# Optimization experiments

Hardware: AMD Instinct MI355X
Metric: run time of the kernel (lower is better)

Reference implementation:

```python
import jax, jax.numpy as jnp
import numpy as np

N = 50000      # nodes
E = 800000     # edges (avg degree 16)
G = 128        # graphs in batch
IN = 128       # in_channels
H = 128        # hidden_dim
C = 10         # num_classes


def setup_inputs() -> dict:
    key = jax.random.key(0)
    ks = jax.random.split(key, 8)
    x = jax.random.normal(ks[0], (N, IN), dtype=jnp.float32)
    edge_index = jax.random.randint(ks[1], (2, E), 0, N)
    edge_attr = jax.random.uniform(ks[2], (E,), dtype=jnp.float32)
    batch = jnp.sort(jax.random.randint(ks[3], (N,), 0, G))
    def glorot(k, fan_in, fan_out):
        return jax.random.normal(k, (fan_in, fan_out), dtype=jnp.float32) / np.float32(np.sqrt(fan_in))
    return {
        "x": x,
        "edge_index": edge_index,
        "edge_attr": edge_attr,
        "batch": batch,
        "W1": glorot(ks[4], IN, H), "b1": jnp.zeros((H,), jnp.float32),
        "W2": glorot(ks[5], H, H), "b2": jnp.zeros((H,), jnp.float32),
        "W3": glorot(ks[6], H, C), "b3": jnp.zeros((C,), jnp.float32),
    }


def gcn_conv(x, src, dst, ew, W, b, n):
    # symmetric GCN normalization (self-loops already appended, weight 1)
    deg = jax.ops.segment_sum(ew, dst, num_segments=n)            # [N]
    dinv = jnp.where(deg > 0, jax.lax.rsqrt(deg), 0.0)
    norm = dinv[src] * ew * dinv[dst]                             # [E+N]
    h = x @ W                                                     # [N, out]
    agg = jax.ops.segment_sum(h[src] * norm[:, None], dst, num_segments=n)
    return agg + b


def reference(x, edge_index, edge_attr, batch, W1, b1, W2, b2, W3, b3):
    n = x.shape[0]
    loop = jnp.arange(n)
    src = jnp.concatenate([edge_index[0], loop])
    dst = jnp.concatenate([edge_index[1], loop])
    ew = jnp.concatenate([edge_attr, jnp.ones((n,), edge_attr.dtype)])
    h = jax.nn.relu(gcn_conv(x, src, dst, ew, W1, b1, n))   # dropout is identity in eval
    h = jax.nn.relu(gcn_conv(h, src, dst, ew, W2, b2, n))
    h = gcn_conv(h, src, dst, ew, W3, b3, n)                 # [N, C]
    # global mean pool over graphs
    sums = jax.ops.segment_sum(h, batch, num_segments=G)     # [G, C]
    cnt = jax.ops.segment_sum(jnp.ones((n,), h.dtype), batch, num_segments=G)
    pooled = sums / jnp.maximum(cnt, 1.0)[:, None]
    return jax.nn.log_softmax(pooled, axis=1)
```

## Files before the change

kernel.cpp:

```cpp
#include <hip/hip_runtime.h>

#define NN 50000
#define NE 800000
#define NG 128
#define DIM 128
#define CO 10
#define CAP 64
#define NB 2048

typedef unsigned long long ull;
typedef unsigned short ushort;
typedef unsigned int uint;
typedef __attribute__((ext_vector_type(8))) short short8;
typedef __attribute__((ext_vector_type(4))) float floatx4;

static __device__ __forceinline__ ushort f2bf(float f) {
    uint u = __float_as_uint(f);
    uint r = (u + 0x7FFF + ((u >> 16) & 1)) >> 16;
    return (ushort)r;
}
#define EWS (1.0f / 65535.0f)
#define DGS (1.0f / 65536.0f)


__global__ void k_ell(const int* __restrict__ src, const int* __restrict__ dst,
                      const float* __restrict__ ew, ull* __restrict__ combo,
                      uint* __restrict__ ell) {
    int e = blockIdx.x * blockDim.x + threadIdx.x;
    if (e >= NE) return;
    int d = dst[e], s = src[e];
    float w = ew[e];
    uint wfix = (uint)__float2uint_rn(w * 65536.0f);
    ull old = atomicAdd(&combo[d], ((ull)wfix << 32) | 1ull);
    int slot = (int)(uint)old;
    if (slot < CAP) {
        uint w16 = (uint)__float2uint_rn(w * 65535.0f);
        ell[(size_t)d * CAP + slot] = (w16 << 16) | (uint)s;
    }
}

__global__ void k_prepw(const float* __restrict__ W1, const float* __restrict__ W2,
                        ushort* __restrict__ wt1, ushort* __restrict__ wt2) {
    int b = blockIdx.x;
    const float* W = (b < 64) ? W1 : W2;
    ushort* Wt = (b < 64) ? wt1 : wt2;
    int i = (b & 63) * 256 + threadIdx.x;
    int k = i >> 7, n = i & 127;
    Wt[n * 128 + k] = f2bf(W[i]);
}

static __device__ __forceinline__ float combo_dinv(ull cb) {
    return rsqrtf(1.0f + (float)(uint)(cb >> 32) * DGS);
}

__global__ __launch_bounds__(256) void k_gemm_mfma(const void* __restrict__ Ain, int abf,
                                                   const ushort* __restrict__ Wt,
                                                   const ull* __restrict__ combo,
                                                   ushort* __restrict__ C, int M) {
    int wave = threadIdx.x >> 6;
    int lane = threadIdx.x & 63;
    int quad = lane >> 4;
    int mcol = lane & 15;
    int r0 = blockIdx.x * 64 + wave * 16;
    int arow = r0 + mcol;
    if (arow >= M) arow = M - 1;
    floatx4 acc[8];
#pragma unroll
    for (int t = 0; t < 8; t++) acc[t] = (floatx4){0.0f, 0.0f, 0.0f, 0.0f};

    const ushort* Ab = (const ushort*)Ain;
    const float*  Af = (const float*)Ain;
#pragma unroll
    for (int kk = 0; kk < 4; kk++) {
        int koff = kk * 32 + quad * 8;
        short8 a;
        if (abf) {
            a = *(const short8*)&Ab[(size_t)arow * 128 + koff];
        } else {
            const float* ap = &Af[(size_t)arow * 128 + koff];
            float4 x0 = *(const float4*)ap;
            float4 x1 = *(const float4*)(ap + 4);
            union { short8 v; ushort u[8]; } ua;
            ua.u[0] = f2bf(x0.x); ua.u[1] = f2bf(x0.y); ua.u[2] = f2bf(x0.z); ua.u[3] = f2bf(x0.w);
            ua.u[4] = f2bf(x1.x); ua.u[5] = f2bf(x1.y); ua.u[6] = f2bf(x1.z); ua.u[7] = f2bf(x1.w);
            a = ua.v;
        }
#pragma unroll
        for (int t = 0; t < 8; t++) {
            short8 b = *(const short8*)&Wt[(size_t)(t * 16 + mcol) * 128 + koff];
            acc[t] = __builtin_amdgcn_mfma_f32_16x16x32_bf16(a, b, acc[t], 0, 0, 0);
        }
    }
#pragma unroll
    for (int reg = 0; reg < 4; reg++) {
        int row = r0 + quad * 4 + reg;
        if (row < M) {
            float di = combo_dinv(combo[row]);
            ushort* cp = &C[(size_t)row * 128];
#pragma unroll
            for (int t = 0; t < 8; t++) cp[t * 16 + mcol] = f2bf(di * acc[t][reg]);
        }
    }
}

__global__ __launch_bounds__(256) void k_gemm10(const ushort* __restrict__ A,
                                                const float* __restrict__ W3,
                                                const ull* __restrict__ combo,
                                                float* __restrict__ C3, int M) {
    __shared__ float Ws[1280];
    int tid = threadIdx.x;
    for (int i = tid; i < 1280; i += 256) Ws[i] = W3[i];
    __syncthreads();
    int col = tid & 15;
    int rloc = tid >> 4;
    int row = blockIdx.x * 16 + rloc;
    if (row >= M || col >= 10) return;
    ull cb = combo[row];
    const ushort* a = &A[(size_t)row * 128];
    float acc = 0.0f;
#pragma unroll
    for (int k = 0; k < 128; k += 4) {
        ushort4 av = *(const ushort4*)&a[k];
        acc += __uint_as_float((uint)av.x << 16) * Ws[(k + 0) * 10 + col];
        acc += __uint_as_float((uint)av.y << 16) * Ws[(k + 1) * 10 + col];
        acc += __uint_as_float((uint)av.z << 16) * Ws[(k + 2) * 10 + col];
        acc += __uint_as_float((uint)av.w << 16) * Ws[(k + 3) * 10 + col];
    }
    C3[(size_t)row * 10 + col] = combo_dinv(cb) * acc;
}

__global__ __launch_bounds__(256) void k_gather128(const ull* __restrict__ combo,
                                                   const uint* __restrict__ ell,
                                                   const ushort* __restrict__ h,
                                                   const float* __restrict__ b,
                                                   ushort* __restrict__ outp) {
    int node = blockIdx.x * 4 + (threadIdx.x >> 6);
    int lane = threadIdx.x & 63;
    if (node >= NN) return;
    ull cb = combo[node];
    int n = min((int)(uint)cb, 63);
    float dg = (float)(uint)(cb >> 32) * DGS;
    int ce; float we;
    if (lane < n) {
        uint rec = ell[(size_t)node * CAP + lane];
        ce = (int)(rec & 0xffffu);
        we = (float)(rec >> 16) * EWS;
    } else {
        ce = node;
        we = (lane == n) ? 1.0f : 0.0f;
    }
    int grp  = lane >> 4;
    int col8 = lane & 15;
    float acc[8];
#pragma unroll
    for (int f = 0; f < 8; f++) acc[f] = 0.0f;
    int nb = (n + 4) >> 2;
    for (int bi = 0; bi < nb; bi++) {
        int idx = (bi << 2) | grp;
        int s = __shfl(ce, idx);
        float w = __shfl(we, idx);
        uint4 p = *(const uint4*)&h[(size_t)s * 128 + col8 * 8];
        acc[0] += w * __uint_as_float(p.x << 16);
        acc[1] += w * __uint_as_float(p.x & 0xffff0000u);
        acc[2] += w * __uint_as_float(p.y << 16);
        acc[3] += w * __uint_as_float(p.y & 0xffff0000u);
        acc[4] += w * __uint_as_float(p.z << 16);
        acc[5] += w * __uint_as_float(p.z & 0xffff0000u);
        acc[6] += w * __uint_as_float(p.w << 16);
        acc[7] += w * __uint_as_float(p.w & 0xffff0000u);
    }
#pragma unroll
    for (int f = 0; f < 8; f++) {
        acc[f] += __shfl_xor(acc[f], 16);
        acc[f] += __shfl_xor(acc[f], 32);
    }
    if (lane < 16) {
        float di = rsqrtf(1.0f + dg);
        union { ushort u[8]; uint4 v; } o;
#pragma unroll
        for (int f = 0; f < 8; f++) {
            float vv = fmaxf(di * acc[f] + b[col8 * 8 + f], 0.0f);
            o.u[f] = f2bf(vv);
        }
        *(uint4*)&outp[(size_t)node * 128 + col8 * 8] = o.v;
    }
}

__global__ __launch_bounds__(256) void k_pool_node(const ull* __restrict__ combo,
                                                   const uint* __restrict__ ell,
                                                   const float* __restrict__ z,
                                                   const int* __restrict__ batch,
                                                   float* __restrict__ partial) {
    __shared__ float ls[NG * CO + NG];
    for (int i = threadIdx.x; i < NG * CO + NG; i += 256) ls[i] = 0.0f;
    __syncthreads();
    int lane = threadIdx.x & 63;
    int gwave = blockIdx.x * 4 + (threadIdx.x >> 6);
    for (int node = gwave; node < NN; node += NB * 4) {
        ull cb = combo[node];
        int n = min((int)(uint)cb, CAP);
        float w = 0.0f; int s = 0;
        if (lane < n) {
            uint rec = ell[(size_t)node * CAP + lane];
            s = (int)(rec & 0xffffu);
            w = (float)(rec >> 16) * EWS;
        } else if (lane == n) {
            s = node;
            w = 1.0f;
        }
        const float* zp = &z[(size_t)s * 10];
        float v[10];
#pragma unroll
        for (int f = 0; f < 10; f++) v[f] = w * zp[f];
#pragma unroll
        for (int off = 32; off; off >>= 1) {
#pragma unroll
            for (int f = 0; f < 10; f++) v[f] += __shfl_down(v[f], off);
        }
        if (lane == 0) {
            int g = batch[node];
            float di = combo_dinv(cb);
            float* lp = &ls[g * 10];
#pragma unroll
            for (int f = 0; f < 10; f++) atomicAdd(&lp[f], di * v[f]);
            atomicAdd(&ls[NG * CO + g], 1.0f);
        }
    }
    __syncthreads();
    float* pb = &partial[(size_t)blockIdx.x * (NG * CO + NG)];
    for (int i = threadIdx.x; i < NG * CO + NG; i += 256) pb[i] = ls[i];
}

__global__ __launch_bounds__(256) void k_pool_final(const float* __restrict__ partial,
                                                    const float* __restrict__ b3,
                                                    float* __restrict__ out) {
    __shared__ float red[4][11];
    int g = blockIdx.x;
    int t = threadIdx.x;
    int lane = t & 63, wv = t >> 6;
    float v[10]; float c = 0.0f;
#pragma unroll
    for (int f = 0; f < 10; f++) v[f] = 0.0f;
    for (int b = t; b < NB; b += 256) {
        const float* pb = &partial[(size_t)b * (NG * CO + NG)];
#pragma unroll
        for (int f = 0; f < 10; f++) v[f] += pb[g * 10 + f];
        c += pb[NG * CO + g];
    }
#pragma unroll
    for (int off = 32; off; off >>= 1) {
#pragma unroll
        for (int f = 0; f < 10; f++) v[f] += __shfl_down(v[f], off);
        c += __shfl_down(c, off);
    }
    if (lane == 0) {
#pragma unroll
        for (int f = 0; f < 10; f++) red[wv][f] = v[f];
        red[wv][10] = c;
    }
    __syncthreads();
    if (t == 0) {
        float p[10], m = -1e30f;
        float cc = red[0][10] + red[1][10] + red[2][10] + red[3][10];
        cc = fmaxf(cc, 1.0f);
#pragma unroll
        for (int f = 0; f < 10; f++) {
            p[f] = (red[0][f] + red[1][f] + red[2][f] + red[3][f]) / cc + b3[f];
            m = fmaxf(m, p[f]);
        }
        float ssum = 0.0f;
#pragma unroll
        for (int f = 0; f < 10; f++) ssum += __expf(p[f] - m);
        float lse = m + __logf(ssum);
#pragma unroll
        for (int f = 0; f < 10; f++) out[g * 10 + f] = p[f] - lse;
    }
}

extern "C" void kernel_launch(void* const* d_in, const int* in_sizes, int n_in,
                              void* d_out, int out_size, void* d_ws, size_t ws_size,
                              hipStream_t stream) {
    const float* x     = (const float*)d_in[0];
    const int*   ei    = (const int*)d_in[1];
    const float* ea    = (const float*)d_in[2];
    const int*   batch = (const int*)d_in[3];
    const float* W1    = (const float*)d_in[4];
    const float* b1    = (const float*)d_in[5];
    const float* W2    = (const float*)d_in[6];
    const float* b2    = (const float*)d_in[7];
    const float* W3    = (const float*)d_in[8];
    const float* b3    = (const float*)d_in[9];
    float* out = (float*)d_out;
    float* ws  = (float*)d_ws;

    const int* esrc = ei;
    const int* edst = ei + NE;

    ushort* hb      = (ushort*)ws;
    ushort* gb      = (ushort*)(ws + 3200000);
    float*  z       = ws + 6400000;
    ull*    combo   = (ull*)(ws + 6900000);
    uint*   ell     = (uint*)(ws + 7000000);
    ushort* wt1     = (ushort*)(ws + 10200000);
    ushort* wt2     = (ushort*)(ws + 10210000);
    float*  partial = (float*)hb;

    hipMemsetAsync(combo, 0, NN * sizeof(ull), stream);
    k_ell<<<(NE + 255) / 256, 256, 0, stream>>>(esrc, edst, ea, combo, ell);
    k_prepw<<<128, 256, 0, stream>>>(W1, W2, wt1, wt2);

    k_gemm_mfma<<<(NN + 63) / 64, 256, 0, stream>>>(x, 0, wt1, combo, hb, NN);
    k_gather128<<<(NN + 3) / 4, 256, 0, stream>>>(combo, ell, hb, b1, gb);

    k_gemm_mfma<<<(NN + 63) / 64, 256, 0, stream>>>(gb, 1, wt2, combo, hb, NN);
    k_gather128<<<(NN + 3) / 4, 256, 0, stream>>>(combo, ell, hb, b2, gb);

    k_gemm10<<<(NN + 15) / 16, 256, 0, stream>>>(gb, W3, combo, z, NN);
    k_pool_node<<<NB, 256, 0, stream>>>(combo, ell, z, batch, partial);
    k_pool_final<<<NG, 256, 0, stream>>>(partial, b3, out);
}
```

Measured before the change: 309.9 us.

## Build ELL adjacency via destination bucketing and per-bucket shared-memory assembly

Replaces the single pass of global 64-bit atomics on per-node counters with two phases. First, edges are binned into 128-node destination buckets, each split into 8 segments. Then one block per bucket assembles the ELL rows, degree sums and counts in LDS and writes them out with coalesced vector stores. The aim is to cut contended scattered global atomics and random ELL writes. In exchange it adds a kernel and an intermediate buffer, and any edge that overflows a fixed segment capacity is silently dropped.

```diff
diff --git a/kernel.cpp b/kernel.cpp
--- a/kernel.cpp
+++ b/kernel.cpp
@@ -8,6 +8,12 @@
 #define CAP 64
 #define NB 2048
 
+#define BKT_SHIFT 7
+#define BKT_NODES 128
+#define NBKT 391
+#define NSEG 8
+#define SEGCAP 448
+
 typedef unsigned long long ull;
 typedef unsigned short ushort;
 typedef unsigned int uint;
@@ -22,21 +28,65 @@
 #define EWS (1.0f / 65535.0f)
 #define DGS (1.0f / 65536.0f)
 
-
-__global__ void k_ell(const int* __restrict__ src, const int* __restrict__ dst,
-                      const float* __restrict__ ew, ull* __restrict__ combo,
-                      uint* __restrict__ ell) {
+__global__ void k_bucket(const int* __restrict__ src, const int* __restrict__ dst,
+                         const float* __restrict__ ew, uint* __restrict__ bcnt,
+                         ull* __restrict__ bkt) {
     int e = blockIdx.x * blockDim.x + threadIdx.x;
     if (e >= NE) return;
     int d = dst[e], s = src[e];
     float w = ew[e];
-    uint wfix = (uint)__float2uint_rn(w * 65536.0f);
-    ull old = atomicAdd(&combo[d], ((ull)wfix << 32) | 1ull);
-    int slot = (int)(uint)old;
-    if (slot < CAP) {
-        uint w16 = (uint)__float2uint_rn(w * 65535.0f);
-        ell[(size_t)d * CAP + slot] = (w16 << 16) | (uint)s;
-    }
+    int b = d >> BKT_SHIFT;
+    int sb = b * NSEG + (blockIdx.x & 7);
+    uint pos = atomicAdd(&bcnt[sb * 16], 1u);
+    if (pos < SEGCAP) {
+        ull rec = ((ull)__float_as_uint(w) << 32)
+                | ((uint)(d & (BKT_NODES - 1)) << 16) | (uint)s;
+        bkt[(size_t)sb * SEGCAP + pos] = rec;
+    }
+}
+
+__global__ __launch_bounds__(256) void k_ellbuild(const uint* __restrict__ bcnt,
+                                                  const ull* __restrict__ bkt,
+                                                  ull* __restrict__ combo,
+                                                  uint* __restrict__ ell) {
+    __shared__ uint  lell[BKT_NODES * CAP];
+    __shared__ uint  lcnt[BKT_NODES];
+    __shared__ float ldeg[BKT_NODES];
+    int b = blockIdx.x, tid = threadIdx.x;
+    for (int i = tid; i < BKT_NODES; i += 256) { lcnt[i] = 0; ldeg[i] = 0.0f; }
+    __syncthreads();
+    for (int seg = 0; seg < NSEG; seg++) {
+        int sb = b * NSEG + seg;
+        uint n = min(bcnt[sb * 16], (uint)SEGCAP);
+        const ull* base = &bkt[(size_t)sb * SEGCAP];
+        for (uint r = tid; r < n; r += 256) {
+            ull rec = base[r];
+            uint lo = (uint)rec;
+            float w = __uint_as_float((uint)(rec >> 32));
+            uint doff = (lo >> 16) & 0xffu;
+            uint s = lo & 0xffffu;
+            uint slot = atomicAdd(&lcnt[doff], 1u);
+            atomicAdd(&ldeg[doff], w);
+            if (slot < CAP) {
+                uint w16 = (uint)__float2uint_rn(w * 65535.0f);
+                lell[doff * CAP + slot] = (w16 << 16) | s;
+            }
+        }
+    }
+    __syncthreads();
+    int node0 = b * BKT_NODES;
+    for (int i = tid; i < BKT_NODES; i += 256) {
+        int node = node0 + i;
+        if (node < NN) {
+            uint dfix = (uint)__float2uint_rn(ldeg[i] * 65536.0f);
+            combo[node] = ((ull)dfix << 32) | (ull)lcnt[i];
+        }
+    }
+    int nvalid = min(NN - node0, BKT_NODES);
+    int nvec = nvalid * CAP / 4;
+    uint4* gdst = (uint4*)&ell[(size_t)node0 * CAP];
+    const uint4* lsrc = (const uint4*)lell;
+    for (int i = tid; i < nvec; i += 256) gdst[i] = lsrc[i];
 }
 
 __global__ void k_prepw(const float* __restrict__ W1, const float* __restrict__ W2,
@@ -304,9 +354,12 @@
     ushort* wt1     = (ushort*)(ws + 10200000);
     ushort* wt2     = (ushort*)(ws + 10210000);
     float*  partial = (float*)hb;
-
-    hipMemsetAsync(combo, 0, NN * sizeof(ull), stream);
-    k_ell<<<(NE + 255) / 256, 256, 0, stream>>>(esrc, edst, ea, combo, ell);
+    ull*    bkt     = (ull*)gb;
+    uint*   bcnt    = (uint*)z;
+
+    hipMemsetAsync(bcnt, 0, (size_t)NBKT * NSEG * 16 * sizeof(uint), stream);
+    k_bucket<<<(NE + 255) / 256, 256, 0, stream>>>(esrc, edst, ea, bcnt, bkt);
+    k_ellbuild<<<NBKT, 256, 0, stream>>>(bcnt, bkt, combo, ell);
     k_prepw<<<128, 256, 0, stream>>>(W1, W2, wt1, wt2);
 
     k_gemm_mfma<<<(NN + 63) / 64, 256, 0, stream>>>(x, 0, wt1, combo, hb, NN);
```

Result: slower. 316.7 us (+2.2%).
